# Kernel tuning notes

Measured on AMD Instinct MI355X. Metric: run time of the kernel, lower is better.

Reference implementation:

```python
import jax, jax.numpy as jnp
import numpy as np

NUM_EXPERTS = 8
TOP_K = 2
MOE_DIM = 2048  # gate/up split point; moe_w13 last dim = 2*MOE_DIM


def setup_inputs() -> dict:
    key = jax.random.key(0)
    k1, k2, k3, k4 = jax.random.split(key, 4)
    B, S, D = 4, 2048, 1024
    x = jax.random.normal(k1, (B, S, D), dtype=jnp.float32)
    moe_router = jax.random.normal(k2, (D, NUM_EXPERTS), dtype=jnp.float32) * 0.02
    moe_w13 = jax.random.normal(k3, (NUM_EXPERTS, D, 2 * MOE_DIM), dtype=jnp.float32) * 0.02
    moe_w2 = jax.random.normal(k4, (NUM_EXPERTS, MOE_DIM, D), dtype=jnp.float32) * 0.02
    return {"x": x, "moe_router": moe_router, "moe_w13": moe_w13, "moe_w2": moe_w2}


def _moe_forward(x, moe_router, moe_w13, moe_w2):
    b, s, d = x.shape
    x_flat = x.reshape(b * s, d)  # [T, D]
    # --- routing ---
    router_logits = jnp.einsum('td,de->te', x_flat, moe_router)
    topk_logits, topk_idx = jax.lax.top_k(router_logits, TOP_K)
    topk_weights = jax.nn.softmax(topk_logits, axis=-1).astype(x.dtype)  # [T, K]
    # --- dispatch: flatten + argsort by expert (grouped layout) ---
    tokens = x_flat.shape[0]
    expert_ids = topk_idx.reshape(tokens * TOP_K)
    dispatch_weights = topk_weights.reshape(tokens * TOP_K)
    sort_idx = jnp.argsort(expert_ids, axis=0)
    token_ids = jnp.arange(tokens * TOP_K, dtype=jnp.int32) // TOP_K
    token_ids_sort = token_ids[sort_idx]
    x_sort = x_flat[token_ids_sort]  # [TK, D]
    w_sort = dispatch_weights[sort_idx].astype(x_flat.dtype)  # [TK]
    group_sizes = jnp.bincount(expert_ids, length=NUM_EXPERTS).astype(jnp.int32)
    # --- grouped GEMM expert FFN (SwiGLU) ---
    w13_out = jax.lax.ragged_dot(x_sort, moe_w13, group_sizes)  # [TK, 2*MOE_DIM]
    gate, up = jnp.split(w13_out, [MOE_DIM], axis=-1)
    hidden = jax.nn.silu(gate) * up
    out_dispatch = jax.lax.ragged_dot(hidden, moe_w2, group_sizes)  # [TK, D]
    # --- combine: weighted scatter-add back to token order ---
    out_flat = jnp.zeros_like(x_flat).at[token_ids_sort].add(
        out_dispatch * w_sort[:, None], mode='drop')
    return out_flat.reshape(b, s, d)


def reference(x, moe_router, moe_w13, moe_w2):
    return _moe_forward(x, moe_router, moe_w13, moe_w2)
```

## Files before the change

kernel.cpp:

```cpp
#include <hip/hip_runtime.h>
#include <stdint.h>

#define NE 8
#define TOKENS 8192
#define DIM 1024
#define HDIM 2048
#define N13 4096
#define CAP 17408
#define CAPT 136

typedef __bf16 bf16x8 __attribute__((ext_vector_type(8)));
typedef __bf16 bf16x4_t __attribute__((ext_vector_type(4)));
typedef float f32x4 __attribute__((ext_vector_type(4)));

#define OFF_XB    ((size_t)0)
#define OFF_W13T  ((size_t)16777216)
#define OFF_W2T   (OFF_W13T + (size_t)67108864)
#define OFF_HID   (OFF_W2T + (size_t)33554432)
#define OFF_TIDX  (OFF_HID + (size_t)71303168)
#define OFF_TW    (OFF_TIDX + (size_t)65536)
#define OFF_TOKID (OFF_TW + (size_t)65536)
#define OFF_ROWW  (OFF_TOKID + (size_t)69632)
#define OFF_CTRL  (OFF_ROWW + (size_t)69632)

__device__ __forceinline__ void async_copy16(const void* gsrc, void* ldst) {
  __builtin_amdgcn_global_load_lds(
      (__attribute__((address_space(1))) void*)((void*)(const_cast<void*>(gsrc))),
      (__attribute__((address_space(3))) void*)ldst, 16, 0, 0);
}

__global__ __launch_bounds__(256) void router_kernel(
    const float* __restrict__ x, const float* __restrict__ rt,
    __bf16* __restrict__ xb, int* __restrict__ tidx, float* __restrict__ tw) {
  __shared__ __align__(16) float xrow[DIM];
  __shared__ double red[4][NE];
  const int t = blockIdx.x;
  const int tid = threadIdx.x;
  const int e = tid & 7, ds = tid >> 3;
  const int w = tid >> 6, l = tid & 63;

  f32x4 v = ((const f32x4*)(x + (size_t)t * DIM))[tid];
  ((f32x4*)xrow)[tid] = v;
  bf16x4_t h;
  h[0] = (__bf16)v[0]; h[1] = (__bf16)v[1]; h[2] = (__bf16)v[2]; h[3] = (__bf16)v[3];
  ((bf16x4_t*)(xb + (size_t)t * DIM))[tid] = h;
  __syncthreads();

  double acc = 0.0;
#pragma unroll
  for (int k = 0; k < 32; k++) {
    int kk = (k + ds) & 31;
    int d = ds * 32 + kk;
    acc += (double)xrow[d] * (double)rt[(size_t)d * NE + e];
  }
  acc += __shfl_xor(acc, 8, 64);
  acc += __shfl_xor(acc, 16, 64);
  acc += __shfl_xor(acc, 32, 64);
  if ((l >> 3) == 0) red[w][e] = acc;
  __syncthreads();
  if (tid == 0) {
    double lg[NE];
#pragma unroll
    for (int q = 0; q < NE; q++) lg[q] = red[0][q] + red[1][q] + red[2][q] + red[3][q];
    int i0 = 0; double m0 = lg[0];
    for (int q = 1; q < NE; q++) if (lg[q] > m0) { m0 = lg[q]; i0 = q; }
    int i1 = -1; double m1 = -1.0e300;
    for (int q = 0; q < NE; q++) { if (q == i0) continue; if (lg[q] > m1) { m1 = lg[q]; i1 = q; } }
    double w0 = 1.0 / (1.0 + exp(m1 - m0));
    tidx[t * 2 + 0] = i0; tidx[t * 2 + 1] = i1;
    tw[t * 2 + 0] = (float)w0; tw[t * 2 + 1] = (float)(1.0 - w0);
  }
}

__global__ __launch_bounds__(256) void histo_kernel(const int* __restrict__ tidx,
                                                    int* __restrict__ ctrl) {
  __shared__ int cnt[NE];
  if (threadIdx.x < NE) cnt[threadIdx.x] = 0;
  __syncthreads();
  int i = blockIdx.x * 256 + threadIdx.x;
  atomicAdd(&cnt[tidx[i]], 1);
  __syncthreads();
  if (threadIdx.x < NE) atomicAdd(&ctrl[threadIdx.x], cnt[threadIdx.x]);
}

__global__ __launch_bounds__(256) void transpose_kernel(
    const float* __restrict__ in, __bf16* __restrict__ outp, int K, int N) {
  __shared__ float tile[32][33];
  const size_t mat = (size_t)K * N;
  const float* ip = in + (size_t)blockIdx.z * mat;
  __bf16* op = outp + (size_t)blockIdx.z * mat;
  int n0 = blockIdx.x * 32, k0 = blockIdx.y * 32;
  int tx = threadIdx.x & 31, ty = threadIdx.x >> 5;
#pragma unroll
  for (int q = 0; q < 4; q++) {
    int yy = ty + q * 8;
    tile[yy][tx] = ip[(size_t)(k0 + yy) * N + n0 + tx];
  }
  __syncthreads();
#pragma unroll
  for (int q = 0; q < 4; q++) {
    int yy = ty + q * 8;
    op[(size_t)(n0 + yy) * K + k0 + tx] = (__bf16)tile[tx][yy];
  }
}

__global__ void scan_pad_kernel(int* __restrict__ ctrl, int* __restrict__ token_id,
                                float* __restrict__ row_w) {
  __shared__ int sseg[NE + 1];
  if (threadIdx.x == 0) {
    int s = 0;
    for (int e = 0; e < NE; e++) {
      sseg[e] = s; ctrl[16 + e] = s;
      int c = ctrl[e];
      s += (c + 127) & ~127;
    }
    sseg[NE] = s; ctrl[16 + NE] = s;
  }
  __syncthreads();
  for (int e = 0; e < NE; e++) {
    int c = ctrl[e];
    int pe = sseg[e + 1] - sseg[e];
    for (int i = c + (int)threadIdx.x; i < pe; i += 256) {
      token_id[sseg[e] + i] = -1;
      row_w[sseg[e] + i] = 0.f;
    }
  }
}

__global__ __launch_bounds__(256) void scatter_kernel(
    const int* __restrict__ tidx, const float* __restrict__ tw,
    int* __restrict__ ctrl, int* __restrict__ token_id, float* __restrict__ row_w) {
  int a = blockIdx.x * 256 + threadIdx.x;
  int e = tidx[a];
  int pos = ctrl[16 + e] + atomicAdd(&ctrl[8 + e], 1);
  token_id[pos] = a >> 1;
  row_w[pos] = tw[a];
}

__global__ __launch_bounds__(256) void gemm1_kernel(
    const __bf16* __restrict__ xb, const __bf16* __restrict__ w13t,
    const int* __restrict__ token_id, const int* __restrict__ ctrl,
    __bf16* __restrict__ hidden) {
  __shared__ __align__(16) __bf16 As[128 * 32];
  __shared__ __align__(16) __bf16 Bs[128 * 32];
  const int* seg = ctrl + 16;
  const int row_base = blockIdx.y * 128;
  if (row_base >= seg[NE]) return;
  int e = 0;
#pragma unroll
  for (int q = 1; q <= 7; q++) if (row_base >= seg[q]) e = q;

  const int g0 = blockIdx.x * 64;
  const int tid = threadIdx.x;
  const int l = tid & 63;
  const int wv = tid >> 6, wr = wv >> 1, wc = wv & 1;
  const int quad = l >> 4, lc = l & 15;

  const int s0 = tid, s1 = tid + 256;
  const int am0 = s0 >> 2, am1 = s1 >> 2;
  const int koff = (tid & 3) * 8;
  int t0 = token_id[row_base + am0]; t0 = t0 < 0 ? 0 : t0;
  int t1 = token_id[row_base + am1]; t1 = t1 < 0 ? 0 : t1;
  const __bf16* ga0 = xb + (size_t)t0 * DIM + koff;
  const __bf16* ga1 = xb + (size_t)t1 * DIM + koff;
  const int gr0 = am0 < 64 ? (g0 + am0) : (2048 + g0 + am0 - 64);
  const int gr1 = am1 < 64 ? (g0 + am1) : (2048 + g0 + am1 - 64);
  const __bf16* wb = w13t + (size_t)e * N13 * DIM;
  const __bf16* gb0 = wb + (size_t)gr0 * DIM + koff;
  const __bf16* gb1 = wb + (size_t)gr1 * DIM + koff;

  const f32x4 fzero = {0.f, 0.f, 0.f, 0.f};
  f32x4 acc[4][4];
#pragma unroll
  for (int i = 0; i < 4; i++)
#pragma unroll
    for (int j = 0; j < 4; j++) acc[i][j] = fzero;

  const bf16x8* Af = (const bf16x8*)As;
  const bf16x8* Bf = (const bf16x8*)Bs;
  const int arow = wr * 64 + lc;
  const int brow0 = wc * 32 + lc;

  for (int kt = 0; kt < DIM; kt += 32) {
    async_copy16(ga0 + kt, As + (size_t)s0 * 8);
    async_copy16(ga1 + kt, As + (size_t)s1 * 8);
    async_copy16(gb0 + kt, Bs + (size_t)s0 * 8);
    async_copy16(gb1 + kt, Bs + (size_t)s1 * 8);
    __syncthreads();
    bf16x8 a[4], b[4];
#pragma unroll
    for (int i = 0; i < 4; i++) a[i] = Af[(arow + i * 16) * 4 + quad];
#pragma unroll
    for (int j = 0; j < 4; j++) {
      int br = (j < 2) ? (brow0 + j * 16) : (64 + brow0 + (j - 2) * 16);
      b[j] = Bf[br * 4 + quad];
    }
#pragma unroll
    for (int i = 0; i < 4; i++)
#pragma unroll
      for (int j = 0; j < 4; j++)
        acc[i][j] = __builtin_amdgcn_mfma_f32_16x16x32_bf16(a[i], b[j], acc[i][j], 0, 0, 0);
    __syncthreads();
  }

#pragma unroll
  for (int i = 0; i < 4; i++) {
#pragma unroll
    for (int jj = 0; jj < 2; jj++) {
      f32x4 g = acc[i][jj];
      f32x4 u = acc[i][jj + 2];
      int col = g0 + wc * 32 + jj * 16 + lc;
#pragma unroll
      for (int r = 0; r < 4; r++) {
        int row = row_base + wr * 64 + i * 16 + quad * 4 + r;
        float gv = g[r], uv = u[r];
        float hh = (gv / (1.0f + __expf(-gv))) * uv;
        hidden[(size_t)row * HDIM + col] = (__bf16)hh;
      }
    }
  }
}

__global__ __launch_bounds__(256) void gemm2_kernel(
    const __bf16* __restrict__ hidden, const __bf16* __restrict__ w2t,
    const int* __restrict__ token_id, const float* __restrict__ row_w,
    const int* __restrict__ ctrl, float* __restrict__ out) {
  __shared__ __align__(16) __bf16 As[128 * 32];
  __shared__ __align__(16) __bf16 Bs[128 * 32];
  const int* seg = ctrl + 16;
  const int row_base = blockIdx.y * 128;
  if (row_base >= seg[NE]) return;
  int e = 0;
#pragma unroll
  for (int q = 1; q <= 7; q++) if (row_base >= seg[q]) e = q;

  const int bn0 = blockIdx.x * 128;
  const int tid = threadIdx.x;
  const int l = tid & 63;
  const int wv = tid >> 6, wr = wv >> 1, wc = wv & 1;
  const int quad = l >> 4, lc = l & 15;

  const int s0 = tid, s1 = tid + 256;
  const int am0 = s0 >> 2, am1 = s1 >> 2;
  const int koff = (tid & 3) * 8;
  const __bf16* ga0 = hidden + (size_t)(row_base + am0) * HDIM + koff;
  const __bf16* ga1 = hidden + (size_t)(row_base + am1) * HDIM + koff;
  const __bf16* wb = w2t + (size_t)e * DIM * HDIM;
  const __bf16* gb0 = wb + (size_t)(bn0 + am0) * HDIM + koff;
  const __bf16* gb1 = wb + (size_t)(bn0 + am1) * HDIM + koff;

  const f32x4 fzero = {0.f, 0.f, 0.f, 0.f};
  f32x4 acc[4][4];
#pragma unroll
  for (int i = 0; i < 4; i++)
#pragma unroll
    for (int j = 0; j < 4; j++) acc[i][j] = fzero;

  const bf16x8* Af = (const bf16x8*)As;
  const bf16x8* Bf = (const bf16x8*)Bs;
  const int arow = wr * 64 + lc;
  const int brow = wc * 64 + lc;

  for (int kt = 0; kt < HDIM; kt += 32) {
    async_copy16(ga0 + kt, As + (size_t)s0 * 8);
    async_copy16(ga1 + kt, As + (size_t)s1 * 8);
    async_copy16(gb0 + kt, Bs + (size_t)s0 * 8);
    async_copy16(gb1 + kt, Bs + (size_t)s1 * 8);
    __syncthreads();
    bf16x8 a[4], b[4];
#pragma unroll
    for (int i = 0; i < 4; i++) a[i] = Af[(arow + i * 16) * 4 + quad];
#pragma unroll
    for (int j = 0; j < 4; j++) b[j] = Bf[(brow + j * 16) * 4 + quad];
#pragma unroll
    for (int i = 0; i < 4; i++)
#pragma unroll
      for (int j = 0; j < 4; j++)
        acc[i][j] = __builtin_amdgcn_mfma_f32_16x16x32_bf16(a[i], b[j], acc[i][j], 0, 0, 0);
    __syncthreads();
  }

#pragma unroll
  for (int i = 0; i < 4; i++) {
    int rbase = row_base + wr * 64 + i * 16 + quad * 4;
    int tok[4]; float wt[4];
#pragma unroll
    for (int r = 0; r < 4; r++) { tok[r] = token_id[rbase + r]; wt[r] = row_w[rbase + r]; }
#pragma unroll
    for (int j = 0; j < 4; j++) {
      int col = bn0 + wc * 64 + j * 16 + lc;
#pragma unroll
      for (int r = 0; r < 4; r++) {
        if (tok[r] >= 0)
          atomicAdd(&out[(size_t)tok[r] * DIM + col], acc[i][j][r] * wt[r]);
      }
    }
  }
}

extern "C" void kernel_launch(void* const* d_in, const int* in_sizes, int n_in,
                              void* d_out, int out_size, void* d_ws, size_t ws_size,
                              hipStream_t stream) {
  const float* x   = (const float*)d_in[0];
  const float* rt  = (const float*)d_in[1];
  const float* w13 = (const float*)d_in[2];
  const float* w2  = (const float*)d_in[3];
  float* out = (float*)d_out;
  char* ws = (char*)d_ws;

  __bf16* xb      = (__bf16*)(ws + OFF_XB);
  __bf16* w13t    = (__bf16*)(ws + OFF_W13T);
  __bf16* w2t     = (__bf16*)(ws + OFF_W2T);
  __bf16* hidden  = (__bf16*)(ws + OFF_HID);
  int*    tidx    = (int*)(ws + OFF_TIDX);
  float*  tw      = (float*)(ws + OFF_TW);
  int*    tokid   = (int*)(ws + OFF_TOKID);
  float*  roww    = (float*)(ws + OFF_ROWW);
  int*    ctrl    = (int*)(ws + OFF_CTRL);

  hipMemsetAsync(out, 0, (size_t)TOKENS * DIM * sizeof(float), stream);
  hipMemsetAsync(ctrl, 0, 128, stream);

  hipLaunchKernelGGL(router_kernel, dim3(TOKENS), dim3(256), 0, stream,
                     x, rt, xb, tidx, tw);
  hipLaunchKernelGGL(transpose_kernel, dim3(N13 / 32, DIM / 32, NE), dim3(256), 0, stream,
                     w13, w13t, DIM, N13);
  hipLaunchKernelGGL(transpose_kernel, dim3(DIM / 32, HDIM / 32, NE), dim3(256), 0, stream,
                     w2, w2t, HDIM, DIM);
  hipLaunchKernelGGL(histo_kernel, dim3(TOKENS * 2 / 256), dim3(256), 0, stream, tidx, ctrl);
  hipLaunchKernelGGL(scan_pad_kernel, dim3(1), dim3(256), 0, stream, ctrl, tokid, roww);
  hipLaunchKernelGGL(scatter_kernel, dim3(TOKENS * 2 / 256), dim3(256), 0, stream,
                     tidx, tw, ctrl, tokid, roww);
  hipLaunchKernelGGL(gemm1_kernel, dim3(HDIM / 64, CAPT), dim3(256), 0, stream,
                     xb, w13t, tokid, ctrl, hidden);
  hipLaunchKernelGGL(gemm2_kernel, dim3(DIM / 128, CAPT), dim3(256), 0, stream,
                     hidden, w2t, tokid, roww, ctrl, out);
}
```

Measured before the change: 732.1 us.

## Replace atomic scatter-add combine with bf16 dispatch buffer and gather combine

GEMM2 now writes its per-row results as bf16 into a dispatch buffer instead of doing fp32 atomicAdds into the output. A new combine kernel gathers each token's two expert rows through a recorded position map and writes the weighted sum directly, which also removes the output memset. The scatter kernel aggregates its atomics per block and records each assignment's position. The weight transpose is rewritten so each thread does strided reads and one 16-byte bf16 store, with no LDS tile. The cost is an extra bf16 intermediate buffer, one more launch, and rounding the expert outputs to bf16 before they are combined.

```diff
diff --git a/kernel.cpp b/kernel.cpp
--- a/kernel.cpp
+++ b/kernel.cpp
@@ -14,14 +14,16 @@
 typedef float f32x4 __attribute__((ext_vector_type(4)));
 
 #define OFF_XB    ((size_t)0)
-#define OFF_W13T  ((size_t)16777216)
-#define OFF_W2T   (OFF_W13T + (size_t)67108864)
-#define OFF_HID   (OFF_W2T + (size_t)33554432)
-#define OFF_TIDX  (OFF_HID + (size_t)71303168)
-#define OFF_TW    (OFF_TIDX + (size_t)65536)
-#define OFF_TOKID (OFF_TW + (size_t)65536)
-#define OFF_ROWW  (OFF_TOKID + (size_t)69632)
-#define OFF_CTRL  (OFF_ROWW + (size_t)69632)
+#define OFF_W13T  (OFF_XB    + (size_t)TOKENS * DIM * 2)
+#define OFF_W2T   (OFF_W13T  + (size_t)NE * N13 * DIM * 2)
+#define OFF_HID   (OFF_W2T   + (size_t)NE * DIM * HDIM * 2)
+#define OFF_DISP  (OFF_HID   + (size_t)CAP * HDIM * 2)
+#define OFF_TIDX  (OFF_DISP  + (size_t)CAP * DIM * 2)
+#define OFF_TW    (OFF_TIDX  + (size_t)TOKENS * 2 * 4)
+#define OFF_POS   (OFF_TW    + (size_t)TOKENS * 2 * 4)
+#define OFF_TOKID (OFF_POS   + (size_t)TOKENS * 2 * 4)
+#define OFF_ROWW  (OFF_TOKID + (size_t)CAP * 4)
+#define OFF_CTRL  (OFF_ROWW  + (size_t)CAP * 4)
 
 __device__ __forceinline__ void async_copy16(const void* gsrc, void* ldst) {
   __builtin_amdgcn_global_load_lds(
@@ -85,23 +87,17 @@
 
 __global__ __launch_bounds__(256) void transpose_kernel(
     const float* __restrict__ in, __bf16* __restrict__ outp, int K, int N) {
-  __shared__ float tile[32][33];
   const size_t mat = (size_t)K * N;
   const float* ip = in + (size_t)blockIdx.z * mat;
   __bf16* op = outp + (size_t)blockIdx.z * mat;
-  int n0 = blockIdx.x * 32, k0 = blockIdx.y * 32;
-  int tx = threadIdx.x & 31, ty = threadIdx.x >> 5;
-#pragma unroll
-  for (int q = 0; q < 4; q++) {
-    int yy = ty + q * 8;
-    tile[yy][tx] = ip[(size_t)(k0 + yy) * N + n0 + tx];
-  }
-  __syncthreads();
-#pragma unroll
-  for (int q = 0; q < 4; q++) {
-    int yy = ty + q * 8;
-    op[(size_t)(n0 + yy) * K + k0 + tx] = (__bf16)tile[tx][yy];
-  }
+  const int tid = threadIdx.x;
+  const int n = blockIdx.x * 64 + (tid >> 2);
+  const int kb = blockIdx.y * 32 + (tid & 3) * 8;
+  bf16x8 o;
+#pragma unroll
+  for (int j = 0; j < 8; j++)
+    o[j] = (__bf16)ip[(size_t)(kb + j) * N + n];
+  *(bf16x8*)(op + (size_t)n * K + kb) = o;
 }
 
 __global__ void scan_pad_kernel(int* __restrict__ ctrl, int* __restrict__ token_id,
@@ -129,12 +125,23 @@
 
 __global__ __launch_bounds__(256) void scatter_kernel(
     const int* __restrict__ tidx, const float* __restrict__ tw,
-    int* __restrict__ ctrl, int* __restrict__ token_id, float* __restrict__ row_w) {
-  int a = blockIdx.x * 256 + threadIdx.x;
+    int* __restrict__ ctrl, int* __restrict__ token_id, float* __restrict__ row_w,
+    int* __restrict__ pos_of) {
+  __shared__ int lcnt[NE];
+  __shared__ int lbase[NE];
+  const int tid = threadIdx.x;
+  if (tid < NE) lcnt[tid] = 0;
+  __syncthreads();
+  int a = blockIdx.x * 256 + tid;
   int e = tidx[a];
-  int pos = ctrl[16 + e] + atomicAdd(&ctrl[8 + e], 1);
+  int rank = atomicAdd(&lcnt[e], 1);
+  __syncthreads();
+  if (tid < NE) lbase[tid] = atomicAdd(&ctrl[8 + tid], lcnt[tid]);
+  __syncthreads();
+  int pos = ctrl[16 + e] + lbase[e] + rank;
   token_id[pos] = a >> 1;
   row_w[pos] = tw[a];
+  pos_of[a] = pos;
 }
 
 __global__ __launch_bounds__(256) void gemm1_kernel(
@@ -223,8 +230,7 @@
 
 __global__ __launch_bounds__(256) void gemm2_kernel(
     const __bf16* __restrict__ hidden, const __bf16* __restrict__ w2t,
-    const int* __restrict__ token_id, const float* __restrict__ row_w,
-    const int* __restrict__ ctrl, float* __restrict__ out) {
+    const int* __restrict__ ctrl, __bf16* __restrict__ disp) {
   __shared__ __align__(16) __bf16 As[128 * 32];
   __shared__ __align__(16) __bf16 Bs[128 * 32];
   const int* seg = ctrl + 16;
@@ -283,19 +289,30 @@
 #pragma unroll
   for (int i = 0; i < 4; i++) {
     int rbase = row_base + wr * 64 + i * 16 + quad * 4;
-    int tok[4]; float wt[4];
-#pragma unroll
-    for (int r = 0; r < 4; r++) { tok[r] = token_id[rbase + r]; wt[r] = row_w[rbase + r]; }
 #pragma unroll
     for (int j = 0; j < 4; j++) {
       int col = bn0 + wc * 64 + j * 16 + lc;
 #pragma unroll
-      for (int r = 0; r < 4; r++) {
-        if (tok[r] >= 0)
-          atomicAdd(&out[(size_t)tok[r] * DIM + col], acc[i][j][r] * wt[r]);
-      }
-    }
-  }
+      for (int r = 0; r < 4; r++)
+        disp[(size_t)(rbase + r) * DIM + col] = (__bf16)acc[i][j][r];
+    }
+  }
+}
+
+__global__ __launch_bounds__(256) void combine_kernel(
+    const __bf16* __restrict__ disp, const int* __restrict__ pos_of,
+    const float* __restrict__ tw, float* __restrict__ out) {
+  const int t = blockIdx.x;
+  const int tid = threadIdx.x;
+  const int p0 = pos_of[t * 2], p1 = pos_of[t * 2 + 1];
+  const float w0 = tw[t * 2], w1 = tw[t * 2 + 1];
+  bf16x4_t d0 = ((const bf16x4_t*)(disp + (size_t)p0 * DIM))[tid];
+  bf16x4_t d1 = ((const bf16x4_t*)(disp + (size_t)p1 * DIM))[tid];
+  f32x4 o;
+#pragma unroll
+  for (int i = 0; i < 4; i++)
+    o[i] = w0 * (float)d0[i] + w1 * (float)d1[i];
+  ((f32x4*)(out + (size_t)t * DIM))[tid] = o;
 }
 
 extern "C" void kernel_launch(void* const* d_in, const int* in_sizes, int n_in,
@@ -312,27 +329,30 @@
   __bf16* w13t    = (__bf16*)(ws + OFF_W13T);
   __bf16* w2t     = (__bf16*)(ws + OFF_W2T);
   __bf16* hidden  = (__bf16*)(ws + OFF_HID);
+  __bf16* disp    = (__bf16*)(ws + OFF_DISP);
   int*    tidx    = (int*)(ws + OFF_TIDX);
   float*  tw      = (float*)(ws + OFF_TW);
+  int*    pos_of  = (int*)(ws + OFF_POS);
   int*    tokid   = (int*)(ws + OFF_TOKID);
   float*  roww    = (float*)(ws + OFF_ROWW);
   int*    ctrl    = (int*)(ws + OFF_CTRL);
 
-  hipMemsetAsync(out, 0, (size_t)TOKENS * DIM * sizeof(float), stream);
   hipMemsetAsync(ctrl, 0, 128, stream);
 
   hipLaunchKernelGGL(router_kernel, dim3(TOKENS), dim3(256), 0, stream,
                      x, rt, xb, tidx, tw);
-  hipLaunchKernelGGL(transpose_kernel, dim3(N13 / 32, DIM / 32, NE), dim3(256), 0, stream,
+  hipLaunchKernelGGL(transpose_kernel, dim3(N13 / 64, DIM / 32, NE), dim3(256), 0, stream,
                      w13, w13t, DIM, N13);
-  hipLaunchKernelGGL(transpose_kernel, dim3(DIM / 32, HDIM / 32, NE), dim3(256), 0, stream,
+  hipLaunchKernelGGL(transpose_kernel, dim3(DIM / 64, HDIM / 32, NE), dim3(256), 0, stream,
                      w2, w2t, HDIM, DIM);
   hipLaunchKernelGGL(histo_kernel, dim3(TOKENS * 2 / 256), dim3(256), 0, stream, tidx, ctrl);
   hipLaunchKernelGGL(scan_pad_kernel, dim3(1), dim3(256), 0, stream, ctrl, tokid, roww);
   hipLaunchKernelGGL(scatter_kernel, dim3(TOKENS * 2 / 256), dim3(256), 0, stream,
-                     tidx, tw, ctrl, tokid, roww);
+                     tidx, tw, ctrl, tokid, roww, pos_of);
   hipLaunchKernelGGL(gemm1_kernel, dim3(HDIM / 64, CAPT), dim3(256), 0, stream,
                      xb, w13t, tokid, ctrl, hidden);
   hipLaunchKernelGGL(gemm2_kernel, dim3(DIM / 128, CAPT), dim3(256), 0, stream,
-                     hidden, w2t, tokid, roww, ctrl, out);
-}
+                     hidden, w2t, ctrl, disp);
+  hipLaunchKernelGGL(combine_kernel, dim3(TOKENS), dim3(256), 0, stream,
+                     disp, pos_of, tw, out);
+}
```

New measurement: 592.1 us. 1.24x faster.
